# Kernel tuning notes

Hardware: AMD Instinct MI355X
Metric: run time of the kernel (lower is better)

Reference implementation:

```python
import jax, jax.numpy as jnp
import numpy as np

E_LAYERS, D_MODEL, D_STATE, D_CONV, DT_RANK, D_FF = 2, 512, 16, 2, 32, 2048
BATCH, SEQ = 16, 512


def layer_norm(x, w, b, eps=1e-5):
    m = x.mean(-1, keepdims=True)
    v = ((x - m) ** 2).mean(-1, keepdims=True)
    return (x - m) / jnp.sqrt(v + eps) * w + b


def mamba(x, in_w, conv_w, conv_b, xproj_w, dt_w, dt_b, A_log, D_skip, out_w):
    # x: [B, L, D]; expand=1 so d_inner == D
    Bsz, L, D = x.shape
    N = A_log.shape[-1]
    R = dt_w.shape[-1]
    xz = x @ in_w.T                      # [B, L, 2D]
    xi, z = jnp.split(xz, 2, axis=-1)
    # causal depthwise conv1d, kernel K
    K = conv_w.shape[-1]
    xp = jnp.pad(xi.transpose(0, 2, 1), ((0, 0), (0, 0), (K - 1, 0)))  # [B, D, L+K-1]
    xc = jax.lax.conv_general_dilated(
        xp, conv_w[:, None, :], (1,), 'VALID',
        dimension_numbers=('NCH', 'OIH', 'NCH'), feature_group_count=D)  # [B, D, L]
    xc = jax.nn.silu(xc.transpose(0, 2, 1) + conv_b)                     # [B, L, D]
    proj = xc @ xproj_w.T                                                # [B, L, R+2N]
    dt, Bm, Cm = jnp.split(proj, [R, R + N], axis=-1)
    dt = jax.nn.softplus(dt @ dt_w.T + dt_b)                             # [B, L, D]
    A = -jnp.exp(A_log)                                                  # [D, N]
    dA = jnp.exp(dt[..., None] * A)                                      # [B, L, D, N]
    dBu = dt[..., None] * Bm[:, :, None, :] * xc[..., None]              # [B, L, D, N]

    def step(h, inp):
        a, b = inp
        h = a * h + b
        return h, h

    _, hs = jax.lax.scan(step, jnp.zeros((Bsz, D, N), x.dtype),
                         (dA.transpose(1, 0, 2, 3), dBu.transpose(1, 0, 2, 3)))
    y = jnp.einsum('lbdn,bln->bld', hs, Cm) + D_skip * xc
    return (y * jax.nn.silu(z)) @ out_w.T


def reference(x, in_w, conv_w, conv_b, xproj_w, dt_w, dt_b, A_log, D_skip, out_w,
              ffn1_w, ffn1_b, ffn2_w, ffn2_b, n1_w, n1_b, n2_w, n2_b, fn_w, fn_b):
    E = in_w.shape[0]
    for e in range(E):
        fwd = mamba(x, in_w[e, 0], conv_w[e, 0], conv_b[e, 0], xproj_w[e, 0],
                    dt_w[e, 0], dt_b[e, 0], A_log[e, 0], D_skip[e, 0], out_w[e, 0])
        xr = jnp.flip(x, axis=1)
        rev = mamba(xr, in_w[e, 1], conv_w[e, 1], conv_b[e, 1], xproj_w[e, 1],
                    dt_w[e, 1], dt_b[e, 1], A_log[e, 1], D_skip[e, 1], out_w[e, 1])
        x = x + fwd + jnp.flip(rev, axis=1)
        x = layer_norm(x, n1_w[e], n1_b[e])
        y = jax.nn.gelu(x @ ffn1_w[e].T + ffn1_b[e], approximate=False)
        y = y @ ffn2_w[e].T + ffn2_b[e]
        x = layer_norm(x + y, n2_w[e], n2_b[e])
    return layer_norm(x, fn_w, fn_b)


def setup_inputs() -> dict:
    key = jax.random.key(0)
    E, D, N, K, R, F = E_LAYERS, D_MODEL, D_STATE, D_CONV, DT_RANK, D_FF
    B, L = BATCH, SEQ
    ks = jax.random.split(key, 12)

    def rn(k, shape, s=0.02):
        return jax.random.normal(k, shape, jnp.float32) * s

    A_log = jnp.tile(jnp.log(jnp.arange(1, N + 1, dtype=jnp.float32)), (E, 2, D, 1))
    return {
        'x': jax.random.normal(ks[0], (B, L, D), jnp.float32),
        'in_w': rn(ks[1], (E, 2, 2 * D, D)),
        'conv_w': rn(ks[2], (E, 2, D, K), 0.5),
        'conv_b': jnp.zeros((E, 2, D), jnp.float32),
        'xproj_w': rn(ks[3], (E, 2, R + 2 * N, D)),
        'dt_w': rn(ks[4], (E, 2, D, R), 0.1),
        'dt_b': rn(ks[5], (E, 2, D), 0.1),
        'A_log': A_log,
        'D_skip': jnp.ones((E, 2, D), jnp.float32),
        'out_w': rn(ks[6], (E, 2, D, D)),
        'ffn1_w': rn(ks[7], (E, F, D)),
        'ffn1_b': jnp.zeros((E, F), jnp.float32),
        'ffn2_w': rn(ks[8], (E, D, F)),
        'ffn2_b': jnp.zeros((E, D), jnp.float32),
        'n1_w': jnp.ones((E, D), jnp.float32),
        'n1_b': jnp.zeros((E, D), jnp.float32),
        'n2_w': jnp.ones((E, D), jnp.float32),
        'n2_b': jnp.zeros((E, D), jnp.float32),
        'fn_w': jnp.ones((D,), jnp.float32),
        'fn_b': jnp.zeros((D,), jnp.float32),
    }
```

## Files before the change

kernel.cpp:

```cpp
#include <hip/hip_runtime.h>

#define BB 16
#define LL 512
#define DD 512
#define ROWS (BB*LL)

typedef unsigned short u16;
typedef __attribute__((ext_vector_type(8))) short short8;
typedef __attribute__((ext_vector_type(4))) float f32x4;
typedef __attribute__((ext_vector_type(4))) unsigned short u16x4;

__device__ __forceinline__ float b2f(u16 u) {
    return __uint_as_float(((unsigned int)u) << 16);
}
__device__ __forceinline__ u16 f2b(float f) {
    unsigned int u = __float_as_uint(f);
    u += 0x7FFFu + ((u >> 16) & 1u);
    return (u16)(u >> 16);
}
__device__ __forceinline__ float ld1(const void* p, size_t i, int f32) {
    return f32 ? ((const float*)p)[i] : b2f(((const u16*)p)[i]);
}
__device__ __forceinline__ float bf_elem(uint4 v, int j) {
    unsigned w = ((const unsigned*)&v)[j >> 1];
    return __uint_as_float((j & 1) ? (w & 0xFFFF0000u) : (w << 16));
}
__device__ __forceinline__ float red16(float x) {
    int v = __float_as_int(x);
    x += __int_as_float(__builtin_amdgcn_update_dpp(0, v, 0xB1, 0xF, 0xF, true));
    v = __float_as_int(x);
    x += __int_as_float(__builtin_amdgcn_update_dpp(0, v, 0x4E, 0xF, 0xF, true));
    v = __float_as_int(x);
    x += __int_as_float(__builtin_amdgcn_update_dpp(0, v, 0x141, 0xF, 0xF, true));
    v = __float_as_int(x);
    x += __int_as_float(__builtin_amdgcn_update_dpp(0, v, 0x140, 0xF, 0xF, true));
    return x;
}

__global__ void detect(const u16* __restrict__ x, int* __restrict__ flag)
{
    __shared__ int s;
    if (threadIdx.x == 0) s = 0;
    __syncthreads();
    u16 v = x[2 * threadIdx.x] & 0x7FFFu;
    if ((v & 0x7F80u) >= 0x5000u) atomicOr(&s, 1);
    __syncthreads();
    if (threadIdx.x == 0) *flag = s;
}

__global__ __launch_bounds__(256)
void cvt_x(const void* __restrict__ X, float* __restrict__ acc, u16* __restrict__ cur,
           const int* __restrict__ flag)
{
    const int f = *flag;
    size_t i = (size_t)blockIdx.x * 256 + threadIdx.x;
    float v = ld1(X, i, f);
    acc[i] = v;
    cur[i] = f2b(v);
}

__global__ __launch_bounds__(256)
void cvt_copy(const void* __restrict__ src, u16* __restrict__ dst, int n,
              const int* __restrict__ flag)
{
    const int f = *flag;
    int i = blockIdx.x * 256 + threadIdx.x;
    if (i < n) dst[i] = f2b(ld1(src, i, f));
}

__global__ __launch_bounds__(256)
void cvt_xp2(const void* __restrict__ xp, u16* __restrict__ dst,
             const int* __restrict__ flag)
{
    const int f = *flag;
    int i = blockIdx.x * 256 + threadIdx.x;
    int e = i >> 17, r = (i >> 10) & 127, c = i & 1023;
    int dir = r >> 6, n = r & 63;
    float v = ((c >> 9) == dir)
        ? ld1(xp, ((size_t)(e*2 + dir)*64 + n)*512 + (c & 511), f) : 0.f;
    dst[i] = f2b(v);
}

__global__ __launch_bounds__(256)
void cvt_dt2(const void* __restrict__ dw, u16* __restrict__ dst,
             const int* __restrict__ flag)
{
    const int f = *flag;
    int i = blockIdx.x * 256 + threadIdx.x;
    int e = i >> 17, r = (i >> 7) & 1023, c = i & 127;
    int dir = r >> 9, d = r & 511;
    float v = 0.f;
    if (dir == 0 && c < 32)
        v = ld1(dw, ((size_t)(e*2)*512 + d)*32 + c, f);
    else if (dir == 1 && c >= 64 && c < 96)
        v = ld1(dw, ((size_t)(e*2 + 1)*512 + d)*32 + (c - 64), f);
    dst[i] = f2b(v);
}

__global__ __launch_bounds__(256)
void cvt_out2(const void* __restrict__ ow, u16* __restrict__ dst,
              const int* __restrict__ flag)
{
    const int f = *flag;
    int i = blockIdx.x * 256 + threadIdx.x;
    int e = i >> 19, rest = i & 524287;
    int d = rest >> 10, c = rest & 1023;
    int dir = c >> 9;
    dst[i] = f2b(ld1(ow, ((size_t)(e*2 + dir)*512 + d)*512 + (c & 511), f));
}

__global__ __launch_bounds__(256)
void acc_init(const u16* __restrict__ x, float* __restrict__ o)
{
    size_t i = (size_t)blockIdx.x * 256 + threadIdx.x;
    o[i] = b2f(x[i]);
}

__global__ __launch_bounds__(256)
void gemm_mfma(const u16* __restrict__ A, const u16* __restrict__ W,
               float* __restrict__ Cf, u16* __restrict__ Cb, u16* __restrict__ CbT,
               int M, int N, int K,
               const void* __restrict__ bias, size_t boff, int act, int accum,
               const int* __restrict__ flag)
{
    const int f = *flag;
    __shared__ u16 As[128][56];
    __shared__ u16 Ws[128][56];
    const int tid  = threadIdx.x;
    const int lane = tid & 63;
    const int wid  = tid >> 6;
    const int wr   = (wid >> 1) * 64;
    const int wc   = (wid & 1) * 64;
    const int row0 = blockIdx.y * 128;
    const int col0 = blockIdx.x * 128;
    const int sr = tid >> 1;
    const int sc = (tid & 1) * 16;
    const int mrow = lane & 15;
    const int kq   = (lane >> 4) * 8;

    f32x4 acc[4][4] = {};
    for (int k0 = 0; k0 < K; k0 += 32) {
        const uint4* ga = (const uint4*)(A + (size_t)(row0 + sr) * K + k0 + sc);
        const uint4* gw = (const uint4*)(W + (size_t)(col0 + sr) * K + k0 + sc);
        uint4 a0 = ga[0], a1 = ga[1];
        uint4 w0 = gw[0], w1 = gw[1];
        *(uint4*)&As[sr][sc]     = a0;
        *(uint4*)&As[sr][sc + 8] = a1;
        *(uint4*)&Ws[sr][sc]     = w0;
        *(uint4*)&Ws[sr][sc + 8] = w1;
        __syncthreads();
        short8 af[4], bf[4];
        #pragma unroll
        for (int mi = 0; mi < 4; ++mi)
            af[mi] = *(const short8*)&As[wr + mi*16 + mrow][kq];
        #pragma unroll
        for (int ni = 0; ni < 4; ++ni)
            bf[ni] = *(const short8*)&Ws[wc + ni*16 + mrow][kq];
        #pragma unroll
        for (int mi = 0; mi < 4; ++mi)
            #pragma unroll
            for (int ni = 0; ni < 4; ++ni)
                acc[mi][ni] = __builtin_amdgcn_mfma_f32_16x16x32_bf16(
                    af[mi], bf[ni], acc[mi][ni], 0, 0, 0);
        __syncthreads();
    }
    const int drow = (lane >> 4) * 4;
    const int dcol = lane & 15;
    #pragma unroll
    for (int mi = 0; mi < 4; ++mi) {
        #pragma unroll
        for (int ni = 0; ni < 4; ++ni) {
            const int rowb = row0 + wr + mi*16 + drow;
            const int col  = col0 + wc + ni*16 + dcol;
            float bv = bias ? ld1(bias, boff + col, f) : 0.f;
            float vv[4];
            #pragma unroll
            for (int r = 0; r < 4; ++r) {
                float v = acc[mi][ni][r] + bv;
                if (act == 1) v = (v > 15.f) ? v : log1pf(__expf(v));
                else if (act == 2) v = 0.5f * v * (1.f + erff(v * 0.70710678118f));
                vv[r] = v;
            }
            if (accum) {
                #pragma unroll
                for (int r = 0; r < 4; ++r)
                    Cf[(size_t)(rowb + r) * N + col] += vv[r];
            } else if (Cf) {
                #pragma unroll
                for (int r = 0; r < 4; ++r)
                    Cf[(size_t)(rowb + r) * N + col] = vv[r];
            } else {
                if (Cb) {
                    #pragma unroll
                    for (int r = 0; r < 4; ++r)
                        Cb[(size_t)(rowb + r) * N + col] = f2b(vv[r]);
                }
                if (CbT) {
                    u16x4 pk;
                    #pragma unroll
                    for (int r = 0; r < 4; ++r) pk[r] = f2b(vv[r]);
                    *(u16x4*)(CbT + (size_t)col * M + rowb) = pk;
                }
            }
        }
    }
}

__global__ __launch_bounds__(256)
void conv_both(u16* __restrict__ xz, const void* __restrict__ cw,
               const void* __restrict__ cb, u16* __restrict__ xc, int e,
               const int* __restrict__ flag)
{
    const int f = *flag;
    int idx = blockIdx.x * 256 + threadIdx.x;
    int row = idx >> 10;
    int c = idx & 1023;
    int dir = c >> 9, d = c & 511;
    int l = row & (LL - 1);
    size_t base = (size_t)row * 2048 + dir * 1024;
    float xcur = b2f(xz[base + d]);
    int dsign = dir ? 1 : -1;
    int ln = l + dsign;
    float xnb = (ln >= 0 && ln < LL) ? b2f(xz[base + dsign*2048 + d]) : 0.f;
    size_t co = (size_t)(e*2 + dir) * 1024 + 2*d;
    float v = ld1(cw, co, f) * xnb + ld1(cw, co + 1, f) * xcur
            + ld1(cb, (size_t)(e*2 + dir)*512 + d, f);
    xc[(size_t)row * 1024 + c] = f2b(v / (1.f + __expf(-v)));
    float z = b2f(xz[base + 512 + d]);
    xz[base + 512 + d] = f2b(z / (1.f + __expf(-z)));
}

__global__ __launch_bounds__(256)
void transp(const u16* __restrict__ src, u16* __restrict__ dst)
{
    __shared__ u16 t[64][72];
    const int c0 = blockIdx.x * 64, r0 = blockIdx.y * 64;
    const int rr = threadIdx.x >> 3, cc = (threadIdx.x & 7) * 8;
    #pragma unroll
    for (int i = 0; i < 2; ++i) {
        uint4 v = *(const uint4*)(src + (size_t)(r0 + rr + i*32) * 1024 + c0 + cc);
        *(uint4*)&t[rr + i*32][cc] = v;
    }
    __syncthreads();
    const int tc = threadIdx.x >> 3, tr = (threadIdx.x & 7) * 8;
    #pragma unroll
    for (int i = 0; i < 2; ++i) {
        u16 tmp[8];
        #pragma unroll
        for (int j = 0; j < 8; ++j) tmp[j] = t[tr + j][tc + i*32];
        *(uint4*)(dst + (size_t)(c0 + tc + i*32) * 8192 + r0 + tr) = *(uint4*)tmp;
    }
}

template<int DIR>
__device__ __forceinline__ void scan_dir(
    const u16* __restrict__ dtp, const u16* __restrict__ xcp,
    const u16* __restrict__ Bp, const u16* __restrict__ Cp,
    const u16* __restrict__ zp, u16* __restrict__ gp,
    float Av, float Dv, int lane)
{
    float h = 0.f;
    int lb = DIR ? (LL - 8) : 0;
    const int stp = DIR ? -8 : 8;
    uint4 d8 = *(const uint4*)(dtp + lb);
    uint4 x8 = *(const uint4*)(xcp + lb);
    uint4 B8 = *(const uint4*)(Bp + lb);
    uint4 C8 = *(const uint4*)(Cp + lb);
    for (int it = 0; it < LL / 8; ++it) {
        const int lbn = lb + stp;
        uint4 nd = d8, nx = x8, nB = B8, nC = C8;
        if (it < LL / 8 - 1) {
            nd = *(const uint4*)(dtp + lbn);
            nx = *(const uint4*)(xcp + lbn);
            nB = *(const uint4*)(Bp + lbn);
            nC = *(const uint4*)(Cp + lbn);
        }
        float keep = 0.f;
        #pragma unroll
        for (int jj = 0; jj < 8; ++jj) {
            const int j = DIR ? (7 - jj) : jj;
            float dtv = bf_elem(d8, j);
            float xv  = bf_elem(x8, j);
            float Bn  = bf_elem(B8, j);
            float Cn  = bf_elem(C8, j);
            h = __expf(dtv * Av) * h + (dtv * xv) * Bn;
            float c = red16(h * Cn) + Dv * xv;
            keep = (lane == j) ? c : keep;
        }
        if (lane < 8) {
            float zs = b2f(zp[(lb + lane) * 2048]);
            gp[(lb + lane) * 1024] = f2b(keep * zs);
        }
        d8 = nd; x8 = nx; B8 = nB; C8 = nC;
        lb = lbn;
    }
}

__global__ __launch_bounds__(256)
void ssm_scan(u16* __restrict__ g, const u16* __restrict__ dtT,
              const u16* __restrict__ xcT, const u16* __restrict__ projT,
              const u16* __restrict__ xz,
              const void* __restrict__ A_log, const void* __restrict__ Dsk,
              int e, const int* __restrict__ flag)
{
    const int f = *flag;
    const int lane = threadIdx.x & 15;
    const int gg = blockIdx.x * 16 + (threadIdx.x >> 4);
    const int dir = gg >> 13;
    const int rem = gg & 8191;
    const int b = rem >> 9, d = rem & 511;
    const int ed = e * 2 + dir;
    const float Av = -__expf(ld1(A_log, (size_t)ed * 8192 + d * 16 + lane, f));
    const float Dv = ld1(Dsk, (size_t)ed * 512 + d, f);
    const int col = dir * 512 + d;
    const size_t tb = (size_t)col * 8192 + b * 512;
    const u16* dtp = dtT + tb;
    const u16* xcp = xcT + tb;
    const u16* Bp  = projT + (size_t)(dir * 64 + 32 + lane) * 8192 + b * 512;
    const u16* Cp  = Bp + (size_t)16 * 8192;
    u16* gp = g + (size_t)b * LL * 1024 + col;
    const u16* zp = xz + (size_t)b * LL * 2048 + dir * 1024 + 512 + d;
    if (dir == 0) scan_dir<0>(dtp, xcp, Bp, Cp, zp, gp, Av, Dv, lane);
    else          scan_dir<1>(dtp, xcp, Bp, Cp, zp, gp, Av, Dv, lane);
}

__global__ __launch_bounds__(256)
void lnorm(const u16* __restrict__ Xb, const float* __restrict__ Xf,
           const void* __restrict__ w, size_t wo, const void* __restrict__ b, size_t bo,
           void* __restrict__ out, int omode, const int* __restrict__ flag)
{
    const int f = *flag;
    int wid = (blockIdx.x * 256 + threadIdx.x) >> 6;
    int lane = threadIdx.x & 63;
    size_t base = (size_t)wid * DD;
    float v[8];
    float s = 0.f;
    #pragma unroll
    for (int i = 0; i < 8; ++i) {
        int c = lane + i*64;
        float t = 0.f;
        if (Xb) t += b2f(Xb[base + c]);
        if (Xf) t += Xf[base + c];
        v[i] = t; s += t;
    }
    #pragma unroll
    for (int off = 32; off > 0; off >>= 1) s += __shfl_xor(s, off);
    float mean = s * (1.f/512.f);
    float var = 0.f;
    #pragma unroll
    for (int i = 0; i < 8; ++i) { float dlt = v[i] - mean; var += dlt*dlt; }
    #pragma unroll
    for (int off = 32; off > 0; off >>= 1) var += __shfl_xor(var, off);
    float rstd = rsqrtf(var * (1.f/512.f) + 1e-5f);
    #pragma unroll
    for (int i = 0; i < 8; ++i) {
        int c = lane + i*64;
        float o = (v[i] - mean) * rstd * ld1(w, wo + c, f) + ld1(b, bo + c, f);
        if (omode && f) ((float*)out)[base + c] = o;
        else            ((u16*)out)[base + c] = f2b(o);
    }
}

extern "C" void kernel_launch(void* const* d_in, const int* in_sizes, int n_in,
                              void* d_out, int out_size, void* d_ws, size_t ws_size,
                              hipStream_t stream)
{
    (void)in_sizes; (void)n_in; (void)out_size; (void)ws_size;
    const void* X       = d_in[0];
    const void* in_w    = d_in[1];
    const void* conv_w  = d_in[2];
    const void* conv_b  = d_in[3];
    const void* xproj_w = d_in[4];
    const void* dt_w    = d_in[5];
    const void* dt_b    = d_in[6];
    const void* A_log   = d_in[7];
    const void* D_skip  = d_in[8];
    const void* out_w   = d_in[9];
    const void* ffn1_w  = d_in[10];
    const void* ffn1_b  = d_in[11];
    const void* ffn2_w  = d_in[12];
    const void* ffn2_b  = d_in[13];
    const void* n1_w    = d_in[14];
    const void* n1_b    = d_in[15];
    const void* n2_w    = d_in[16];
    const void* n2_b    = d_in[17];
    const void* fn_w    = d_in[18];
    const void* fn_b    = d_in[19];

    char* p = (char*)d_ws;
    float* acc   = (float*)(p);
    u16*   cur   = (u16*)(p + 16777216);
    u16*   xz    = (u16*)(p + 25165824);
    u16*   xc    = (u16*)(p + 58720256);
    u16*   dtT   = (u16*)(p + 58720256);
    u16*   g     = (u16*)(p + 75497472);
    u16*   proj  = (u16*)(p + 92274688);
    int*   flag  = (int*)(p + 94371840);
    u16*   wbf   = (u16*)(p + 94375936);
    u16*   xcT   = (u16*)(p + 110104576);
    u16*   projT = (u16*)(p + 126881792);
    u16*   ffh   = xz;
    float* y2    = (float*)xc;
    u16*   x1    = g;
    const size_t W_IN  = 0;
    const size_t W_XP  = 2097152;
    const size_t W_DT  = 2359296;
    const size_t W_OUT = 2621440;
    const size_t W_FF1 = 3670016;
    const size_t W_FF2 = 5767168;

    detect<<<1, 512, 0, stream>>>((const u16*)X, flag);
    cvt_x<<<ROWS*DD/256, 256, 0, stream>>>(X, acc, cur, flag);
    cvt_copy<<<2097152/256, 256, 0, stream>>>(in_w,   wbf + W_IN,  2097152, flag);
    cvt_copy<<<2097152/256, 256, 0, stream>>>(ffn1_w, wbf + W_FF1, 2097152, flag);
    cvt_copy<<<2097152/256, 256, 0, stream>>>(ffn2_w, wbf + W_FF2, 2097152, flag);
    cvt_xp2<<<262144/256, 256, 0, stream>>>(xproj_w, wbf + W_XP, flag);
    cvt_dt2<<<262144/256, 256, 0, stream>>>(dt_w, wbf + W_DT, flag);
    cvt_out2<<<1048576/256, 256, 0, stream>>>(out_w, wbf + W_OUT, flag);

    for (int e = 0; e < 2; ++e) {
        size_t eo = (size_t)e * 512;
        if (e == 1)
            acc_init<<<ROWS*DD/256, 256, 0, stream>>>(cur, acc);
        gemm_mfma<<<dim3(16,64), 256, 0, stream>>>(
            cur, wbf + W_IN + (size_t)e*1048576, nullptr, xz, nullptr,
            ROWS, 2048, 512, nullptr, 0, 0, 0, flag);
        conv_both<<<ROWS*1024/256, 256, 0, stream>>>(xz, conv_w, conv_b, xc, e, flag);
        transp<<<dim3(16,128), 256, 0, stream>>>(xc, xcT);
        gemm_mfma<<<dim3(1,64), 256, 0, stream>>>(
            xc, wbf + W_XP + (size_t)e*131072, nullptr, proj, projT,
            ROWS, 128, 1024, nullptr, 0, 0, 0, flag);
        gemm_mfma<<<dim3(8,64), 256, 0, stream>>>(
            proj, wbf + W_DT + (size_t)e*131072, nullptr, nullptr, dtT,
            ROWS, 1024, 128, dt_b, (size_t)e*1024, 1, 0, flag);
        ssm_scan<<<1024, 256, 0, stream>>>(g, dtT, xcT, projT, xz,
                                           A_log, D_skip, e, flag);
        gemm_mfma<<<dim3(4,64), 256, 0, stream>>>(
            g, wbf + W_OUT + (size_t)e*524288, acc, nullptr, nullptr,
            ROWS, 512, 1024, nullptr, 0, 0, 1, flag);
        lnorm<<<2048, 256, 0, stream>>>(nullptr, acc, n1_w, eo, n1_b, eo, x1, 0, flag);
        gemm_mfma<<<dim3(16,64), 256, 0, stream>>>(
            x1, wbf + W_FF1 + (size_t)e*1048576, nullptr, ffh, nullptr,
            ROWS, 2048, 512, ffn1_b, (size_t)e*2048, 2, 0, flag);
        gemm_mfma<<<dim3(4,64), 256, 0, stream>>>(
            ffh, wbf + W_FF2 + (size_t)e*1048576, y2, nullptr, nullptr,
            ROWS, 512, 2048, ffn2_b, eo, 0, 0, flag);
        lnorm<<<2048, 256, 0, stream>>>(x1, y2, n2_w, eo, n2_b, eo, cur, 0, flag);
    }
    lnorm<<<2048, 256, 0, stream>>>(cur, nullptr, fn_w, 0, fn_b, 0, d_out, 1, flag);
}
```

Baseline: 1.176 ms.

## Load GEMM tiles directly into LDS and double-buffer scan prefetch

The GEMM tile staging now uses global_load_lds, which writes straight from global memory into shared memory without going through registers. Because of that, the padded LDS rows are shrunk to an unpadded 32-wide layout, which can bring back bank conflicts on the MFMA fragment reads. The SSM scan loop is restructured to process two 8-step chunks per iteration with two prefetch buffers, so loads run two chunks ahead of their use. The aim is to hide memory latency in the serial scan and to cut register and VALU overhead in the GEMM load path.

Result: slower. 1.304 ms (+10.9%).

```diff
diff --git a/kernel.cpp b/kernel.cpp
--- a/kernel.cpp
+++ b/kernel.cpp
@@ -36,6 +36,11 @@
     x += __int_as_float(__builtin_amdgcn_update_dpp(0, v, 0x140, 0xF, 0xF, true));
     return x;
 }
+__device__ __forceinline__ void gld16(const u16* g, u16* l) {
+    __builtin_amdgcn_global_load_lds(
+        (const __attribute__((address_space(1))) unsigned int*)g,
+        (__attribute__((address_space(3))) unsigned int*)l, 16, 0, 0);
+}
 
 __global__ void detect(const u16* __restrict__ x, int* __restrict__ flag)
 {
@@ -124,8 +129,8 @@
                const int* __restrict__ flag)
 {
     const int f = *flag;
-    __shared__ u16 As[128][56];
-    __shared__ u16 Ws[128][56];
+    __shared__ u16 As[128][32];
+    __shared__ u16 Ws[128][32];
     const int tid  = threadIdx.x;
     const int lane = tid & 63;
     const int wid  = tid >> 6;
@@ -133,35 +138,35 @@
     const int wc   = (wid & 1) * 64;
     const int row0 = blockIdx.y * 128;
     const int col0 = blockIdx.x * 128;
-    const int sr = tid >> 1;
-    const int sc = (tid & 1) * 16;
     const int mrow = lane & 15;
     const int kq   = (lane >> 4) * 8;
+    const int srow = wid * 32 + (lane >> 2);
+    const int scol = (lane & 3) * 8;
+    const u16* gA = A + (size_t)(row0 + srow) * K + scol;
+    const u16* gW = W + (size_t)(col0 + srow) * K + scol;
+    u16* lA = &As[wid * 32][0];
+    u16* lW = &Ws[wid * 32][0];
 
     f32x4 acc[4][4] = {};
     for (int k0 = 0; k0 < K; k0 += 32) {
-        const uint4* ga = (const uint4*)(A + (size_t)(row0 + sr) * K + k0 + sc);
-        const uint4* gw = (const uint4*)(W + (size_t)(col0 + sr) * K + k0 + sc);
-        uint4 a0 = ga[0], a1 = ga[1];
-        uint4 w0 = gw[0], w1 = gw[1];
-        *(uint4*)&As[sr][sc]     = a0;
-        *(uint4*)&As[sr][sc + 8] = a1;
-        *(uint4*)&Ws[sr][sc]     = w0;
-        *(uint4*)&Ws[sr][sc + 8] = w1;
+        gld16(gA + k0,                  lA);
+        gld16(gA + k0 + (size_t)16 * K, lA + 512);
+        gld16(gW + k0,                  lW);
+        gld16(gW + k0 + (size_t)16 * K, lW + 512);
         __syncthreads();
-        short8 af[4], bf[4];
+        short8 af[4], bfr[4];
         #pragma unroll
         for (int mi = 0; mi < 4; ++mi)
             af[mi] = *(const short8*)&As[wr + mi*16 + mrow][kq];
         #pragma unroll
         for (int ni = 0; ni < 4; ++ni)
-            bf[ni] = *(const short8*)&Ws[wc + ni*16 + mrow][kq];
+            bfr[ni] = *(const short8*)&Ws[wc + ni*16 + mrow][kq];
         #pragma unroll
         for (int mi = 0; mi < 4; ++mi)
             #pragma unroll
             for (int ni = 0; ni < 4; ++ni)
                 acc[mi][ni] = __builtin_amdgcn_mfma_f32_16x16x32_bf16(
-                    af[mi], bf[ni], acc[mi][ni], 0, 0, 0);
+                    af[mi], bfr[ni], acc[mi][ni], 0, 0, 0);
         __syncthreads();
     }
     const int drow = (lane >> 4) * 4;
@@ -253,6 +258,30 @@
 }
 
 template<int DIR>
+__device__ __forceinline__ void chunk8(const uint4& d8, const uint4& x8,
+    const uint4& B8, const uint4& C8, int lb,
+    const u16* __restrict__ zp, u16* __restrict__ gp,
+    float Av, float Dv, float& h, int lane)
+{
+    float keep = 0.f;
+    #pragma unroll
+    for (int jj = 0; jj < 8; ++jj) {
+        const int j = DIR ? (7 - jj) : jj;
+        float dtv = bf_elem(d8, j);
+        float xv  = bf_elem(x8, j);
+        float Bn  = bf_elem(B8, j);
+        float Cn  = bf_elem(C8, j);
+        h = __expf(dtv * Av) * h + (dtv * xv) * Bn;
+        float c = red16(h * Cn) + Dv * xv;
+        keep = (lane == j) ? c : keep;
+    }
+    if (lane < 8) {
+        float zs = b2f(zp[(lb + lane) * 2048]);
+        gp[(lb + lane) * 1024] = f2b(keep * zs);
+    }
+}
+
+template<int DIR>
 __device__ __forceinline__ void scan_dir(
     const u16* __restrict__ dtp, const u16* __restrict__ xcp,
     const u16* __restrict__ Bp, const u16* __restrict__ Cp,
@@ -260,39 +289,27 @@
     float Av, float Dv, int lane)
 {
     float h = 0.f;
+    const int stp = DIR ? -8 : 8;
     int lb = DIR ? (LL - 8) : 0;
-    const int stp = DIR ? -8 : 8;
-    uint4 d8 = *(const uint4*)(dtp + lb);
-    uint4 x8 = *(const uint4*)(xcp + lb);
-    uint4 B8 = *(const uint4*)(Bp + lb);
-    uint4 C8 = *(const uint4*)(Cp + lb);
-    for (int it = 0; it < LL / 8; ++it) {
-        const int lbn = lb + stp;
-        uint4 nd = d8, nx = x8, nB = B8, nC = C8;
-        if (it < LL / 8 - 1) {
-            nd = *(const uint4*)(dtp + lbn);
-            nx = *(const uint4*)(xcp + lbn);
-            nB = *(const uint4*)(Bp + lbn);
-            nC = *(const uint4*)(Cp + lbn);
+    uint4 dP = *(const uint4*)(dtp + lb), xP = *(const uint4*)(xcp + lb);
+    uint4 BP = *(const uint4*)(Bp + lb),  CP = *(const uint4*)(Cp + lb);
+    const int l1 = lb + stp;
+    uint4 dQ = *(const uint4*)(dtp + l1), xQ = *(const uint4*)(xcp + l1);
+    uint4 BQ = *(const uint4*)(Bp + l1),  CQ = *(const uint4*)(Cp + l1);
+    for (int it = 0; it < LL/8; it += 2) {
+        chunk8<DIR>(dP, xP, BP, CP, lb, zp, gp, Av, Dv, h, lane);
+        {
+            int ln = (it + 2 < LL/8) ? lb + 2*stp : lb;
+            dP = *(const uint4*)(dtp + ln); xP = *(const uint4*)(xcp + ln);
+            BP = *(const uint4*)(Bp + ln);  CP = *(const uint4*)(Cp + ln);
         }
-        float keep = 0.f;
-        #pragma unroll
-        for (int jj = 0; jj < 8; ++jj) {
-            const int j = DIR ? (7 - jj) : jj;
-            float dtv = bf_elem(d8, j);
-            float xv  = bf_elem(x8, j);
-            float Bn  = bf_elem(B8, j);
-            float Cn  = bf_elem(C8, j);
-            h = __expf(dtv * Av) * h + (dtv * xv) * Bn;
-            float c = red16(h * Cn) + Dv * xv;
-            keep = (lane == j) ? c : keep;
+        chunk8<DIR>(dQ, xQ, BQ, CQ, lb + stp, zp, gp, Av, Dv, h, lane);
+        {
+            int ln = (it + 3 < LL/8) ? lb + 3*stp : lb;
+            dQ = *(const uint4*)(dtp + ln); xQ = *(const uint4*)(xcp + ln);
+            BQ = *(const uint4*)(Bp + ln);  CQ = *(const uint4*)(Cp + ln);
         }
-        if (lane < 8) {
-            float zs = b2f(zp[(lb + lane) * 2048]);
-            gp[(lb + lane) * 1024] = f2b(keep * zs);
-        }
-        d8 = nd; x8 = nx; B8 = nB; C8 = nC;
-        lb = lbn;
+        lb += 2*stp;
     }
 }
 
```
